# Optimization experiments

Measured on AMD Instinct MI355X. Metric: run time of the kernel, lower is better.

## Reference

```python
import jax, jax.numpy as jnp
import numpy as np
from jax import lax

B = 32768
L_DNA = 103   # -> 96 conv outputs with filter 8
L_PROT = 103
FD = 8
FP = 8
CHUNK = 3
DIMS = ('NCHW', 'OIHW', 'NCHW')


def setup_inputs() -> dict:
    key = jax.random.key(0)
    k1, k2, k3, k4, k5 = jax.random.split(key, 5)
    dna = jax.random.uniform(k1, (B, 1, 4, L_DNA), dtype=jnp.float32)
    prot = jax.random.uniform(k2, (B, 1, 21, L_PROT), dtype=jnp.float32)
    w_dna = jax.random.normal(k3, (1, 1, 4, FD), dtype=jnp.float32) * 0.2
    w_prot = jax.random.normal(k4, (1, 1, 21, FP), dtype=jnp.float32) * 0.1
    kw, kb = jax.random.split(k5)
    w_lin = jax.random.normal(kw, (2, 96), dtype=jnp.float32) * 0.1
    b_lin = jax.random.normal(kb, (2,), dtype=jnp.float32) * 0.01
    return {"dna": dna, "prot": prot, "w_dna": w_dna, "w_prot": w_prot,
            "w_lin": w_lin, "b_lin": b_lin}


def reference(dna, prot, w_dna, w_prot, w_lin, b_lin):
    bsz = dna.shape[0]
    # conv (full-height kernel, single channel) + relu -> (B,1,1,96)
    d = jax.nn.relu(lax.conv_general_dilated(dna, w_dna, (1, 1), 'VALID',
                                             dimension_numbers=DIMS))
    p = jax.nn.relu(lax.conv_general_dilated(prot, w_prot, (1, 1), 'VALID',
                                             dimension_numbers=DIMS))
    L = d.shape[-1]  # 96; equal lengths -> pad_sequence is a no-op
    d = d.reshape(bsz, L)
    p = p.reshape(bsz, L)
    n_chunks = L // CHUNK  # 32
    # torch.stack(torch.chunk(x, n, dim=1)) -> (n_chunks, B, CHUNK),
    # then a raw reshape to (B, n_chunks, CHUNK) as in the original
    sd = jnp.transpose(d.reshape(bsz, n_chunks, CHUNK), (1, 0, 2)).reshape(bsz, n_chunks, CHUNK)
    sp = jnp.transpose(p.reshape(bsz, n_chunks, CHUNK), (1, 0, 2)).reshape(bsz, n_chunks, CHUNK)
    # scaled dot-product attention: q=sp, k=v=sd
    scale = 1.0 / jnp.sqrt(jnp.float32(CHUNK))
    logits = jnp.einsum('bqd,bkd->bqk', sp, sd) * scale
    attn = jax.nn.softmax(logits, axis=-1)
    out = jnp.einsum('bqk,bkd->bqd', attn, sd)  # (B, n_chunks, CHUNK)
    out = out.reshape(bsz, 1, n_chunks * CHUNK)  # (B,1,96)
    return out @ w_lin.T + b_lin  # (B,1,2)
```

## Files before the change

### kernel.cpp

```cpp
#include <hip/hip_runtime.h>


constexpr int NB      = 32;
constexpr int THREADS = 256;
constexpr int NBLOCKS = 1024;

__global__ __launch_bounds__(THREADS, 4)
void fused_matx(const float* __restrict__ dna,
                const float* __restrict__ prot,
                const float* __restrict__ wdna,
                const float* __restrict__ wprot,
                const float* __restrict__ wlin,
                const float* __restrict__ blin,
                float* __restrict__ out)
{
    __shared__ __align__(16) float s_stage[NB * 132];
    __shared__ float4 s_d4[32 * 40];
    __shared__ float2 s_red[128];

    const int tid = threadIdx.x;
    const int j   = blockIdx.x;

    const int cs = tid >> 3;
    const int xb = tid & 7;

    const int pp  = tid & 127;
    const int s0  = tid >> 7;
    const int ppc = (pp < 103) ? pp : 102;
    const int a0d = s0 * 412  + ppc;
    const int a0p = s0 * 2163 + ppc;
    const int l0  = s0 * 132  + pp;

    const float* dbase = dna  + (size_t)j * NB * 412;
    const float* pbase = prot + (size_t)j * NB * 2163;

    float pfA[16], pfB[16];

    auto pf_dna = [&](int c, float (&pf)[16]) {
        const float* pa = dbase + c * 103 + a0d;
#pragma unroll
        for (int k = 0; k < 16; ++k) pf[k] = pa[824 * k];
    };
    auto pf_prot = [&](int c, float (&pf)[16]) {
        const float* pa = pbase + c * 103 + a0p;
#pragma unroll
        for (int k = 0; k < 16; ++k) pf[k] = pa[4326 * k];
    };
    auto wr = [&](float (&pf)[16]) {
#pragma unroll
        for (int k = 0; k < 16; ++k) s_stage[l0 + 264 * k] = pf[k];
    };
    auto conv8 = [&](const float* __restrict__ wsrc, int c, float (&acc)[12]) {
        float w[8];
#pragma unroll
        for (int f = 0; f < 8; ++f) w[f] = wsrc[c * 8 + f];
        float in[20];
        const float4* sp = reinterpret_cast<const float4*>(&s_stage[cs * 132 + 12 * xb]);
#pragma unroll
        for (int u = 0; u < 5; ++u) {
            float4 v = sp[u];
            in[4*u+0] = v.x; in[4*u+1] = v.y; in[4*u+2] = v.z; in[4*u+3] = v.w;
        }
#pragma unroll
        for (int f = 0; f < 8; ++f)
#pragma unroll
            for (int o = 0; o < 12; ++o)
                acc[o] = fmaf(in[o + f], w[f], acc[o]);
    };

    float dacc[12];
#pragma unroll
    for (int o = 0; o < 12; ++o) dacc[o] = 0.f;

    pf_dna(0, pfA);
    wr(pfA); pf_dna(1, pfB); __syncthreads(); conv8(wdna, 0, dacc); __syncthreads();
    wr(pfB); pf_dna(2, pfA); __syncthreads(); conv8(wdna, 1, dacc); __syncthreads();
    wr(pfA); pf_dna(3, pfB); __syncthreads(); conv8(wdna, 2, dacc); __syncthreads();
    wr(pfB); pf_prot(0, pfA); __syncthreads(); conv8(wdna, 3, dacc); __syncthreads();

#pragma unroll
    for (int u = 0; u < 4; ++u) {
        float4 v;
        v.x = fmaxf(dacc[3*u+0], 0.f);
        v.y = fmaxf(dacc[3*u+1], 0.f);
        v.z = fmaxf(dacc[3*u+2], 0.f);
        v.w = 0.f;
        s_d4[(4 * xb + u) * 40 + cs + xb] = v;
    }

    float pacc[12];
#pragma unroll
    for (int o = 0; o < 12; ++o) pacc[o] = 0.f;

    for (int q = 0; q < 20; q += 2) {
        wr(pfA); pf_prot(q + 1, pfB); __syncthreads(); conv8(wprot, q,     pacc); __syncthreads();
        wr(pfB); pf_prot(q + 2, pfA); __syncthreads(); conv8(wprot, q + 1, pacc); __syncthreads();
    }
    wr(pfA); __syncthreads(); conv8(wprot, 20, pacc);

    const float4* dp = s_d4 + 161 * xb;
    float wl0[3], wl1[3];
#pragma unroll
    for (int t = 0; t < 3; ++t) {
        wl0[t] = wlin[3 * cs + t];
        wl1[t] = wlin[96 + 3 * cs + t];
    }
    const float escale = 0.5773502691896258f;

#pragma unroll
    for (int it = 0; it < 4; ++it) {
        const float q0 = fmaxf(pacc[3*it+0], 0.f);
        const float q1 = fmaxf(pacc[3*it+1], 0.f);
        const float q2 = fmaxf(pacc[3*it+2], 0.f);

        float sum = 0.f, v0 = 0.f, v1 = 0.f, v2 = 0.f;
#pragma unroll
        for (int r = 0; r < 32; ++r) {
            float4 dv = dp[40 * it + r];
            float l = fmaf(q0, dv.x, fmaf(q1, dv.y, q2 * dv.z));
            float e = __expf(l * escale);
            sum += e;
            v0 = fmaf(e, dv.x, v0);
            v1 = fmaf(e, dv.y, v1);
            v2 = fmaf(e, dv.z, v2);
        }
        const float inv = 1.f / sum;
        float o0 = (wl0[0] * v0 + wl0[1] * v1 + wl0[2] * v2) * inv;
        float o1 = (wl1[0] * v0 + wl1[1] * v1 + wl1[2] * v2) * inv;
        o0 += __shfl_xor(o0, 8);  o1 += __shfl_xor(o1, 8);
        o0 += __shfl_xor(o0, 16); o1 += __shfl_xor(o1, 16);
        o0 += __shfl_xor(o0, 32); o1 += __shfl_xor(o1, 32);
        if ((tid & 56) == 0)
            s_red[(tid >> 6) * 32 + 4 * xb + it] = make_float2(o0, o1);
    }
    __syncthreads();

    if (tid < 32) {
        float2 a = s_red[tid], b = s_red[32 + tid], c = s_red[64 + tid], d = s_red[96 + tid];
        float2 r;
        r.x = a.x + b.x + c.x + d.x + blin[0];
        r.y = a.y + b.y + c.y + d.y + blin[1];
        *reinterpret_cast<float2*>(&out[(size_t)((tid << 10) + j) * 2]) = r;
    }
}

extern "C" void kernel_launch(void* const* d_in, const int* in_sizes, int n_in,
                              void* d_out, int out_size, void* d_ws, size_t ws_size,
                              hipStream_t stream) {
    const float* dna   = (const float*)d_in[0];
    const float* prot  = (const float*)d_in[1];
    const float* wdna  = (const float*)d_in[2];
    const float* wprot = (const float*)d_in[3];
    const float* wlin  = (const float*)d_in[4];
    const float* blin  = (const float*)d_in[5];
    float* out = (float*)d_out;

    fused_matx<<<NBLOCKS, THREADS, 0, stream>>>(dna, prot, wdna, wprot, wlin, blin, out);
}
```

Measured before the change: 68.35 us.

## Stage conv inputs with direct global-to-LDS loads into double-buffered shared memory

```diff
diff --git a/kernel.cpp b/kernel.cpp
--- a/kernel.cpp
+++ b/kernel.cpp
@@ -1,9 +1,13 @@
 #include <hip/hip_runtime.h>
+#include <stdint.h>
 
 
 constexpr int NB      = 32;
 constexpr int THREADS = 256;
 constexpr int NBLOCKS = 1024;
+
+#define AS_GLB const __attribute__((address_space(1))) void
+#define AS_LDS __attribute__((address_space(3))) void
 
 __global__ __launch_bounds__(THREADS, 4)
 void fused_matx(const float* __restrict__ dna,
@@ -14,48 +18,40 @@
                 const float* __restrict__ blin,
                 float* __restrict__ out)
 {
-    __shared__ __align__(16) float s_stage[NB * 132];
-    __shared__ float4 s_d4[32 * 40];
+    __shared__ __align__(16) float s_mem[2 * 4224];
     __shared__ float2 s_red[128];
 
     const int tid = threadIdx.x;
     const int j   = blockIdx.x;
 
-    const int cs = tid >> 3;
-    const int xb = tid & 7;
+    const int cs   = tid >> 3;
+    const int xb   = tid & 7;
+    const int pp   = tid & 127;
+    const int s0   = tid >> 7;
+    const int half = (tid >> 6) & 1;
+    const int ppc  = (pp < 103) ? pp : 102;
 
-    const int pp  = tid & 127;
-    const int s0  = tid >> 7;
-    const int ppc = (pp < 103) ? pp : 102;
-    const int a0d = s0 * 412  + ppc;
-    const int a0p = s0 * 2163 + ppc;
-    const int l0  = s0 * 132  + pp;
+    const float* gd0 = dna  + (size_t)j * NB * 412  + s0 * 412  + ppc;
+    const float* gp0 = prot + (size_t)j * NB * 2163 + s0 * 2163 + ppc;
 
-    const float* dbase = dna  + (size_t)j * NB * 412;
-    const float* pbase = prot + (size_t)j * NB * 2163;
+    float* const l0a = &s_mem[       s0 * 132 + half * 64];
+    float* const l0b = &s_mem[4224 + s0 * 132 + half * 64];
+    const float* const bufA = &s_mem[0];
+    const float* const bufB = &s_mem[4224];
 
-    float pfA[16], pfB[16];
-
-    auto pf_dna = [&](int c, float (&pf)[16]) {
-        const float* pa = dbase + c * 103 + a0d;
+    auto stage = [&](const float* g0, const int gstr, float* const l0) {
 #pragma unroll
-        for (int k = 0; k < 16; ++k) pf[k] = pa[824 * k];
+        for (int k = 0; k < 16; ++k)
+            __builtin_amdgcn_global_load_lds((AS_GLB*)(g0 + (size_t)k * gstr),
+                                             (AS_LDS*)(l0 + k * 264), 4, 0, 0);
     };
-    auto pf_prot = [&](int c, float (&pf)[16]) {
-        const float* pa = pbase + c * 103 + a0p;
-#pragma unroll
-        for (int k = 0; k < 16; ++k) pf[k] = pa[4326 * k];
-    };
-    auto wr = [&](float (&pf)[16]) {
-#pragma unroll
-        for (int k = 0; k < 16; ++k) s_stage[l0 + 264 * k] = pf[k];
-    };
-    auto conv8 = [&](const float* __restrict__ wsrc, int c, float (&acc)[12]) {
+    auto conv8 = [&](const float* buf, const float* __restrict__ wsrc, int c,
+                     float (&acc)[12]) {
         float w[8];
 #pragma unroll
         for (int f = 0; f < 8; ++f) w[f] = wsrc[c * 8 + f];
         float in[20];
-        const float4* sp = reinterpret_cast<const float4*>(&s_stage[cs * 132 + 12 * xb]);
+        const float4* sp = reinterpret_cast<const float4*>(buf + cs * 132 + 12 * xb);
 #pragma unroll
         for (int u = 0; u < 5; ++u) {
             float4 v = sp[u];
@@ -68,16 +64,36 @@
                 acc[o] = fmaf(in[o + f], w[f], acc[o]);
     };
 
-    float dacc[12];
+    float dacc[12], pacc[12];
 #pragma unroll
-    for (int o = 0; o < 12; ++o) dacc[o] = 0.f;
+    for (int o = 0; o < 12; ++o) { dacc[o] = 0.f; pacc[o] = 0.f; }
 
-    pf_dna(0, pfA);
-    wr(pfA); pf_dna(1, pfB); __syncthreads(); conv8(wdna, 0, dacc); __syncthreads();
-    wr(pfB); pf_dna(2, pfA); __syncthreads(); conv8(wdna, 1, dacc); __syncthreads();
-    wr(pfA); pf_dna(3, pfB); __syncthreads(); conv8(wdna, 2, dacc); __syncthreads();
-    wr(pfB); pf_prot(0, pfA); __syncthreads(); conv8(wdna, 3, dacc); __syncthreads();
+    stage(gp0, 4326, l0a);
+    __syncthreads();
+    for (int c = 0; c < 20; c += 2) {
+        stage(gp0 + (c + 1) * 103, 4326, l0b);
+        conv8(bufA, wprot, c, pacc);
+        __syncthreads();
+        stage(gp0 + (c + 2) * 103, 4326, l0a);
+        conv8(bufB, wprot, c + 1, pacc);
+        __syncthreads();
+    }
+    stage(gd0, 824, l0b);
+    conv8(bufA, wprot, 20, pacc);
+    __syncthreads();
+    stage(gd0 + 103, 824, l0a);
+    conv8(bufB, wdna, 0, dacc);
+    __syncthreads();
+    stage(gd0 + 206, 824, l0b);
+    conv8(bufA, wdna, 1, dacc);
+    __syncthreads();
+    stage(gd0 + 309, 824, l0a);
+    conv8(bufB, wdna, 2, dacc);
+    __syncthreads();
+    conv8(bufA, wdna, 3, dacc);
+    __syncthreads();
 
+    float4* const s_d4 = reinterpret_cast<float4*>(s_mem);
 #pragma unroll
     for (int u = 0; u < 4; ++u) {
         float4 v;
@@ -87,16 +103,7 @@
         v.w = 0.f;
         s_d4[(4 * xb + u) * 40 + cs + xb] = v;
     }
-
-    float pacc[12];
-#pragma unroll
-    for (int o = 0; o < 12; ++o) pacc[o] = 0.f;
-
-    for (int q = 0; q < 20; q += 2) {
-        wr(pfA); pf_prot(q + 1, pfB); __syncthreads(); conv8(wprot, q,     pacc); __syncthreads();
-        wr(pfB); pf_prot(q + 2, pfA); __syncthreads(); conv8(wprot, q + 1, pacc); __syncthreads();
-    }
-    wr(pfA); __syncthreads(); conv8(wprot, 20, pacc);
+    __syncthreads();
 
     const float4* dp = s_d4 + 161 * xb;
     float wl0[3], wl1[3];
```

New measurement: 70.75 us, median of 2. +3.5%, slower.

## Give each wavefront private LDS staging to drop block-wide barriers in conv

Applied to the files above, without the earlier changes.

```diff
diff --git a/kernel.cpp b/kernel.cpp
--- a/kernel.cpp
+++ b/kernel.cpp
@@ -14,48 +14,55 @@
                 const float* __restrict__ blin,
                 float* __restrict__ out)
 {
-    __shared__ __align__(16) float s_stage[NB * 132];
+    __shared__ __align__(16) float s_stage[4 * 832];
     __shared__ float4 s_d4[32 * 40];
     __shared__ float2 s_red[128];
 
-    const int tid = threadIdx.x;
-    const int j   = blockIdx.x;
+    const int tid  = threadIdx.x;
+    const int j    = blockIdx.x;
+    const int w    = tid >> 6;
+    const int lane = tid & 63;
+    const int cs   = tid >> 3;
+    const int xb   = tid & 7;
 
-    const int cs = tid >> 3;
-    const int xb = tid & 7;
+    int gP[13], gD[13], lOf[13];
+#pragma unroll
+    for (int k = 0; k < 13; ++k) {
+        int i = lane + 64 * k;
+        if (i > 823) i = 823;
+        int r = i / 103;
+        int p = i - r * 103;
+        gP[k]  = r * 2163 + p;
+        gD[k]  = r * 412  + p;
+        lOf[k] = w * 832 + r * 104 + p;
+    }
 
-    const int pp  = tid & 127;
-    const int s0  = tid >> 7;
-    const int ppc = (pp < 103) ? pp : 102;
-    const int a0d = s0 * 412  + ppc;
-    const int a0p = s0 * 2163 + ppc;
-    const int l0  = s0 * 132  + pp;
+    const float* dbase = dna  + (size_t)(j * NB + 8 * w) * 412;
+    const float* pbase = prot + (size_t)(j * NB + 8 * w) * 2163;
 
-    const float* dbase = dna  + (size_t)j * NB * 412;
-    const float* pbase = prot + (size_t)j * NB * 2163;
+    float pfA[13], pfB[13];
 
-    float pfA[16], pfB[16];
-
-    auto pf_dna = [&](int c, float (&pf)[16]) {
-        const float* pa = dbase + c * 103 + a0d;
+    auto ldP = [&](int c, float (&pf)[13]) {
+        const float* b = pbase + c * 103;
 #pragma unroll
-        for (int k = 0; k < 16; ++k) pf[k] = pa[824 * k];
+        for (int k = 0; k < 13; ++k) pf[k] = b[gP[k]];
     };
-    auto pf_prot = [&](int c, float (&pf)[16]) {
-        const float* pa = pbase + c * 103 + a0p;
+    auto ldD = [&](int c, float (&pf)[13]) {
+        const float* b = dbase + c * 103;
 #pragma unroll
-        for (int k = 0; k < 16; ++k) pf[k] = pa[4326 * k];
+        for (int k = 0; k < 13; ++k) pf[k] = b[gD[k]];
     };
-    auto wr = [&](float (&pf)[16]) {
+    auto st = [&](float (&pf)[13]) {
 #pragma unroll
-        for (int k = 0; k < 16; ++k) s_stage[l0 + 264 * k] = pf[k];
+        for (int k = 0; k < 13; ++k) s_stage[lOf[k]] = pf[k];
     };
     auto conv8 = [&](const float* __restrict__ wsrc, int c, float (&acc)[12]) {
-        float w[8];
+        float wv[8];
 #pragma unroll
-        for (int f = 0; f < 8; ++f) w[f] = wsrc[c * 8 + f];
+        for (int f = 0; f < 8; ++f) wv[f] = wsrc[c * 8 + f];
         float in[20];
-        const float4* sp = reinterpret_cast<const float4*>(&s_stage[cs * 132 + 12 * xb]);
+        const float4* sp = reinterpret_cast<const float4*>(
+            &s_stage[w * 832 + (cs & 7) * 104 + 12 * xb]);
 #pragma unroll
         for (int u = 0; u < 5; ++u) {
             float4 v = sp[u];
@@ -65,18 +72,25 @@
         for (int f = 0; f < 8; ++f)
 #pragma unroll
             for (int o = 0; o < 12; ++o)
-                acc[o] = fmaf(in[o + f], w[f], acc[o]);
+                acc[o] = fmaf(in[o + f], wv[f], acc[o]);
     };
 
-    float dacc[12];
+    float dacc[12], pacc[12];
 #pragma unroll
-    for (int o = 0; o < 12; ++o) dacc[o] = 0.f;
+    for (int o = 0; o < 12; ++o) { dacc[o] = 0.f; pacc[o] = 0.f; }
 
-    pf_dna(0, pfA);
-    wr(pfA); pf_dna(1, pfB); __syncthreads(); conv8(wdna, 0, dacc); __syncthreads();
-    wr(pfB); pf_dna(2, pfA); __syncthreads(); conv8(wdna, 1, dacc); __syncthreads();
-    wr(pfA); pf_dna(3, pfB); __syncthreads(); conv8(wdna, 2, dacc); __syncthreads();
-    wr(pfB); pf_prot(0, pfA); __syncthreads(); conv8(wdna, 3, dacc); __syncthreads();
+    ldP(0, pfA);
+    ldP(1, pfB); st(pfA); conv8(wprot, 0, pacc);
+    for (int c = 2; c < 20; c += 2) {
+        ldP(c,     pfA); st(pfB); conv8(wprot, c - 1, pacc);
+        ldP(c + 1, pfB); st(pfA); conv8(wprot, c,     pacc);
+    }
+    ldP(20, pfA); st(pfB); conv8(wprot, 19, pacc);
+    ldD(0,  pfB); st(pfA); conv8(wprot, 20, pacc);
+    ldD(1,  pfA); st(pfB); conv8(wdna, 0, dacc);
+    ldD(2,  pfB); st(pfA); conv8(wdna, 1, dacc);
+    ldD(3,  pfA); st(pfB); conv8(wdna, 2, dacc);
+                  st(pfA); conv8(wdna, 3, dacc);
 
 #pragma unroll
     for (int u = 0; u < 4; ++u) {
@@ -87,16 +101,7 @@
         v.w = 0.f;
         s_d4[(4 * xb + u) * 40 + cs + xb] = v;
     }
-
-    float pacc[12];
-#pragma unroll
-    for (int o = 0; o < 12; ++o) pacc[o] = 0.f;
-
-    for (int q = 0; q < 20; q += 2) {
-        wr(pfA); pf_prot(q + 1, pfB); __syncthreads(); conv8(wprot, q,     pacc); __syncthreads();
-        wr(pfB); pf_prot(q + 2, pfA); __syncthreads(); conv8(wprot, q + 1, pacc); __syncthreads();
-    }
-    wr(pfA); __syncthreads(); conv8(wprot, 20, pacc);
+    __syncthreads();
 
     const float4* dp = s_d4 + 161 * xb;
     float wl0[3], wl1[3];
@@ -131,7 +136,7 @@
         o0 += __shfl_xor(o0, 16); o1 += __shfl_xor(o1, 16);
         o0 += __shfl_xor(o0, 32); o1 += __shfl_xor(o1, 32);
         if ((tid & 56) == 0)
-            s_red[(tid >> 6) * 32 + 4 * xb + it] = make_float2(o0, o1);
+            s_red[w * 32 + 4 * xb + it] = make_float2(o0, o1);
     }
     __syncthreads();
 
```

Measured after the change: 63.87 us. 6.6% less time.
